# Kernel tuning notes

Hardware: AMD Instinct MI355X
Metric: run time of the kernel (lower is better)

Reference implementation:

```python
import jax, jax.numpy as jnp
import numpy as np

B, TQ, TK = 4, 128, 512
DQ = DK = DV = H = 1024


def setup_inputs() -> dict:
    key = jax.random.key(0)
    ks = jax.random.split(key, 7)
    s = 0.05  # keep tanh out of saturation
    return {
        "query": jax.random.normal(ks[0], (B, TQ, DQ), dtype=jnp.float32),
        "key": jax.random.normal(ks[1], (B, TK, DK), dtype=jnp.float32),
        "value": jax.random.normal(ks[2], (B, TK, DV), dtype=jnp.float32),
        "Wq": jax.random.normal(ks[3], (DQ, H), dtype=jnp.float32) * s,
        "bq": jax.random.normal(ks[4], (H,), dtype=jnp.float32) * s,
        "Wk": jax.random.normal(ks[5], (DK, H), dtype=jnp.float32) * s,
        "v": jax.random.normal(ks[6], (H,), dtype=jnp.float32) * s,
    }


def reference(query, key, value, Wq, bq, Wk, v):
    # additive (Bahdanau) attention
    wq = jnp.einsum("bqd,dh->bqh", query, Wq) + bq      # [B,Tq,H]
    uh = jnp.einsum("bkd,dh->bkh", key, Wk)             # [B,Tk,H]
    # broadcast add -> [B,Tq,Tk,H], tanh, project to scalar score
    scores = jnp.einsum("bqkh,h->bqk",
                        jnp.tanh(wq[:, :, None, :] + uh[:, None, :, :]), v)
    attn = jax.nn.softmax(scores, axis=-1)              # [B,Tq,Tk]
    h = jnp.einsum("bqk,bkv->bqv", attn, value)         # [B,Tq,Dv]
    return h, attn
```

## Files before the change

kernel.cpp:

```cpp
#include <hip/hip_runtime.h>
#include <hip/hip_bf16.h>

typedef float f32x4 __attribute__((ext_vector_type(4)));
typedef short s16x8 __attribute__((ext_vector_type(8)));
typedef short s16x4 __attribute__((ext_vector_type(4)));

#define NB  4
#define NTQ 128
#define NTK 512
#define NH  1024

__device__ __forceinline__ unsigned short f2bf(float x) {
    unsigned u = __builtin_bit_cast(unsigned, x);
    u += 0x7FFFu + ((u >> 16) & 1u);
    return (unsigned short)(u >> 16);
}

#define K2E  2.8853900817779268f

#define GLD16(gp, lp) __builtin_amdgcn_global_load_lds( \
    (const __attribute__((address_space(1))) unsigned int*)(gp), \
    (__attribute__((address_space(3))) unsigned int*)(lp), 16, 0, 0)

__global__ __launch_bounds__(256) void prep_kernel(
    const float* __restrict__ Q, const float* __restrict__ K,
    const float* __restrict__ Wq, const float* __restrict__ Wk,
    const float* __restrict__ value,
    short* __restrict__ Qb, short* __restrict__ Kb,
    short* __restrict__ WqT, short* __restrict__ WkT, short* __restrict__ valT)
{
    const int t = threadIdx.x, bx = blockIdx.x;
    if (bx < 2560) {
        const float* src; short* dst; size_t off;
        if (bx < 512) { src = Q; dst = Qb; off = (size_t)bx * 1024 + t * 4; }
        else          { src = K; dst = Kb; off = (size_t)(bx - 512) * 1024 + t * 4; }
        const float4 vv = *(const float4*)(src + off);
        s16x4 o = { (short)f2bf(vv.x), (short)f2bf(vv.y),
                    (short)f2bf(vv.z), (short)f2bf(vv.w) };
        *(s16x4*)(dst + off) = o;
        return;
    }
    __shared__ float tile[32][33];
    const float* src; short* dst; int R, C, r0, c0;
    if (bx < 3584)      { const int i = bx - 2560; src = Wq; dst = WqT; C = 1024; R = 1024; r0 = (i >> 5) * 32; c0 = (i & 31) * 32; }
    else if (bx < 4608) { const int i = bx - 3584; src = Wk; dst = WkT; C = 1024; R = 1024; r0 = (i >> 5) * 32; c0 = (i & 31) * 32; }
    else {
        const int i = bx - 4608, b = i >> 9, rr = i & 511;
        src = value + (size_t)b * 512 * 1024; dst = valT + (size_t)b * 1024 * 512;
        C = 1024; R = 512; r0 = (rr >> 5) * 32; c0 = (rr & 31) * 32;
    }
    const int lr = t >> 3, lc = (t & 7) * 4;
    {
        const float4 vv = *(const float4*)(src + (size_t)(r0 + lr) * C + c0 + lc);
        tile[lr][lc + 0] = vv.x; tile[lr][lc + 1] = vv.y;
        tile[lr][lc + 2] = vv.z; tile[lr][lc + 3] = vv.w;
    }
    __syncthreads();
    s16x4 o = { (short)f2bf(tile[lc + 0][lr]), (short)f2bf(tile[lc + 1][lr]),
                (short)f2bf(tile[lc + 2][lr]), (short)f2bf(tile[lc + 3][lr]) };
    *(s16x4*)(dst + (size_t)(c0 + lr) * R + r0 + lc) = o;
}

__global__ __launch_bounds__(256) void mm_kernel(
    const short* __restrict__ Qb, const short* __restrict__ Kb,
    const short* __restrict__ WqT, const short* __restrict__ WkT,
    const float* __restrict__ bq,
    float* __restrict__ Ea_out, float* __restrict__ EbT)
{
    __shared__ short lds[2][2][128][64];
    const int t = threadIdx.x, bx = blockIdx.x;
    const bool g1 = bx < 32;
    const short *A, *B; int m0, n0;
    if (g1) { A = Qb; B = WqT; m0 = (bx >> 3) * 128;        n0 = (bx & 7) * 128; }
    else    { const int i = bx - 32; A = Kb; B = WkT; m0 = (i >> 3) * 128; n0 = (i & 7) * 128; }
    A += (size_t)m0 * 1024; B += (size_t)n0 * 1024;

    f32x4 acc[4][4];
    #pragma unroll
    for (int i = 0; i < 4; ++i)
        #pragma unroll
        for (int j = 0; j < 4; ++j) acc[i][j] = f32x4{0.f, 0.f, 0.f, 0.f};

    const int lane = t & 63, wid = t >> 6;
    const int wr = wid >> 1, wc = wid & 1;
    const int fr = lane & 15, fko = (lane >> 4) * 16;

    #define STAGE_MM(buf, k0) do {                                              \
        _Pragma("unroll")                                                       \
        for (int it = 0; it < 4; ++it) {                                        \
            const int idx = it * 256 + t;                                       \
            const int row = idx >> 3, c16 = idx & 7;                            \
            const int sc = c16 ^ (row & 7);                                     \
            GLD16(A + (size_t)row * 1024 + (k0) + sc * 8,                       \
                  &lds[buf][0][0][0] + idx * 8);                                \
            GLD16(B + (size_t)row * 1024 + (k0) + sc * 8,                       \
                  &lds[buf][1][0][0] + idx * 8);                                \
        }                                                                       \
    } while (0)

    #define COMPUTE_MM(buf) do {                                                \
        _Pragma("unroll")                                                       \
        for (int kk = 0; kk < 2; ++kk) {                                        \
            s16x8 af[4], bfv[4];                                                \
            _Pragma("unroll")                                                   \
            for (int i = 0; i < 4; ++i) {                                       \
                const int rowA = wr * 64 + i * 16 + fr;                         \
                int offA = rowA * 128 + kk * 64 + fko; offA ^= (rowA & 7) << 4; \
                af[i] = *(const s16x8*)((const char*)&lds[buf][0][0][0] + offA);\
                const int rowB = wc * 64 + i * 16 + fr;                         \
                int offB = rowB * 128 + kk * 64 + fko; offB ^= (rowB & 7) << 4; \
                bfv[i] = *(const s16x8*)((const char*)&lds[buf][1][0][0] + offB);\
            }                                                                   \
            _Pragma("unroll")                                                   \
            for (int mi = 0; mi < 4; ++mi)                                      \
                _Pragma("unroll")                                               \
                for (int ni = 0; ni < 4; ++ni)                                  \
                    acc[mi][ni] = __builtin_amdgcn_mfma_f32_16x16x32_bf16(      \
                                      af[mi], bfv[ni], acc[mi][ni], 0, 0, 0);   \
        }                                                                       \
    } while (0)

    STAGE_MM(0, 0);
    __syncthreads();
    int cur = 0;
    for (int s = 0; s < 15; ++s) {
        STAGE_MM(cur ^ 1, (s + 1) * 64);
        COMPUTE_MM(cur);
        __syncthreads();
        cur ^= 1;
    }
    COMPUTE_MM(cur);

    const int row0 = (lane >> 4) * 4;
    if (g1) {
        #pragma unroll
        for (int ni = 0; ni < 4; ++ni) {
            const int n = n0 + wc * 64 + ni * 16 + fr;
            const float bias = bq[n];
            #pragma unroll
            for (int mi = 0; mi < 4; ++mi) {
                const int m = m0 + wr * 64 + mi * 16 + row0;
                #pragma unroll
                for (int j = 0; j < 4; ++j)
                    Ea_out[(size_t)(m + j) * 1024 + n] =
                        __builtin_amdgcn_exp2f(K2E * (acc[mi][ni][j] + bias));
            }
        }
    } else {
        #pragma unroll
        for (int mi = 0; mi < 4; ++mi) {
            const int m = m0 + wr * 64 + mi * 16 + row0;
            const int b = m >> 9, kk = m & 511;
            #pragma unroll
            for (int ni = 0; ni < 4; ++ni) {
                const int n = n0 + wc * 64 + ni * 16 + fr;
                f32x4 ev;
                #pragma unroll
                for (int j = 0; j < 4; ++j)
                    ev[j] = __builtin_amdgcn_exp2f(K2E * acc[mi][ni][j]);
                *(f32x4*)&EbT[((size_t)b * 1024 + n) * 512 + kk] = ev;
            }
        }
    }
    #undef STAGE_MM
    #undef COMPUTE_MM
}

__global__ __launch_bounds__(512) void scores_partial(
    const float* __restrict__ EbT, const float* __restrict__ Ea,
    const float* __restrict__ v, float* __restrict__ partial)
{
    __shared__ float s_ea[128][8];
    __shared__ float s_v[128];
    const int t = threadIdx.x, bx = blockIdx.x;
    const int hc = bx & 7, bq8 = bx >> 3;
    const int b = bq8 >> 4, q8 = bq8 & 15;
    const int bq0 = b * 128 + q8 * 8, h0 = hc * 128;

    if (t < 128) {
        #pragma unroll
        for (int q = 0; q < 8; ++q)
            s_ea[t][q] = Ea[(size_t)(bq0 + q) * 1024 + h0 + t];
        s_v[t] = v[h0 + t];
    }
    __syncthreads();

    const float* up = EbT + ((size_t)b * 1024 + h0) * 512 + t;
    float a[8] = {0.f, 0.f, 0.f, 0.f, 0.f, 0.f, 0.f, 0.f};
    #pragma unroll 4
    for (int hh = 0; hh < 128; ++hh) {
        const float eb = up[(size_t)hh * 512];
        const float vv = s_v[hh];
        #pragma unroll
        for (int q = 0; q < 8; ++q) {
            const float r = __builtin_amdgcn_rcpf(__builtin_fmaf(s_ea[hh][q], eb, 1.0f));
            a[q] = __builtin_fmaf(vv, r, a[q]);
        }
    }
    #pragma unroll
    for (int q = 0; q < 8; ++q)
        partial[((size_t)(bq0 + q) * 8 + hc) * 512 + t] = a[q];
}

__global__ __launch_bounds__(512) void softmax_kernel(
    const float* __restrict__ partial, float* __restrict__ attn_out,
    short* __restrict__ attnb)
{
    __shared__ float s_red[16];
    const int t = threadIdx.x, bqi = blockIdx.x;
    const float* p = partial + (size_t)bqi * 4096;
    float zs = 0.f;
    #pragma unroll
    for (int j = 0; j < 8; ++j) zs += p[j * 512 + t];
    const float z = -2.0f * zs;

    const int lane = t & 63, wid = t >> 6;
    float m = z;
    #pragma unroll
    for (int off = 32; off > 0; off >>= 1)
        m = fmaxf(m, __shfl_xor(m, off, 64));
    if (lane == 0) s_red[wid] = m;
    __syncthreads();
    if (t < 64) {
        float mm = (t < 8) ? s_red[t] : -3.0e38f;
        #pragma unroll
        for (int off = 4; off > 0; off >>= 1)
            mm = fmaxf(mm, __shfl_xor(mm, off, 64));
        if (t == 0) s_red[8] = mm;
    }
    __syncthreads();
    const float pr = __expf(z - s_red[8]);
    float s = pr;
    #pragma unroll
    for (int off = 32; off > 0; off >>= 1)
        s += __shfl_xor(s, off, 64);
    if (lane == 0) s_red[wid] = s;
    __syncthreads();
    if (t < 64) {
        float ss = (t < 8) ? s_red[t] : 0.f;
        #pragma unroll
        for (int off = 4; off > 0; off >>= 1)
            ss += __shfl_xor(ss, off, 64);
        if (t == 0) s_red[9] = ss;
    }
    __syncthreads();
    const float attn = pr * (1.0f / s_red[9]);
    attn_out[(size_t)bqi * 512 + t] = attn;
    attnb[(size_t)bqi * 512 + t] = (short)f2bf(attn);
}

__global__ __launch_bounds__(256) void pv_gemm(
    const short* __restrict__ attnb, const short* __restrict__ valT,
    float* __restrict__ outh)
{
    __shared__ short lds[2][2][128][64];
    const int t = threadIdx.x, bx = blockIdx.x;
    const int b = bx >> 3, nt = bx & 7;
    const int n0 = nt * 128;
    const short* A = attnb + (size_t)b * 128 * 512;
    const short* B = valT + (size_t)b * 1024 * 512 + (size_t)n0 * 512;

    f32x4 acc[4][4];
    #pragma unroll
    for (int i = 0; i < 4; ++i)
        #pragma unroll
        for (int j = 0; j < 4; ++j) acc[i][j] = f32x4{0.f, 0.f, 0.f, 0.f};

    const int lane = t & 63, wid = t >> 6;
    const int wr = wid >> 1, wc = wid & 1;
    const int fr = lane & 15, fko = (lane >> 4) * 16;

    #define STAGE_PV(buf, k0) do {                                              \
        _Pragma("unroll")                                                       \
        for (int it = 0; it < 4; ++it) {                                        \
            const int idx = it * 256 + t;                                       \
            const int row = idx >> 3, c16 = idx & 7;                            \
            const int sc = c16 ^ (row & 7);                                     \
            GLD16(A + (size_t)row * 512 + (k0) + sc * 8,                        \
                  &lds[buf][0][0][0] + idx * 8);                                \
            GLD16(B + (size_t)row * 512 + (k0) + sc * 8,                        \
                  &lds[buf][1][0][0] + idx * 8);                                \
        }                                                                       \
    } while (0)

    #define COMPUTE_PV(buf) do {                                                \
        _Pragma("unroll")                                                       \
        for (int kk = 0; kk < 2; ++kk) {                                        \
            s16x8 af[4], bfv[4];                                                \
            _Pragma("unroll")                                                   \
            for (int i = 0; i < 4; ++i) {                                       \
                const int rowA = wr * 64 + i * 16 + fr;                         \
                int offA = rowA * 128 + kk * 64 + fko; offA ^= (rowA & 7) << 4; \
                af[i] = *(const s16x8*)((const char*)&lds[buf][0][0][0] + offA);\
                const int rowB = wc * 64 + i * 16 + fr;                         \
                int offB = rowB * 128 + kk * 64 + fko; offB ^= (rowB & 7) << 4; \
                bfv[i] = *(const s16x8*)((const char*)&lds[buf][1][0][0] + offB);\
            }                                                                   \
            _Pragma("unroll")                                                   \
            for (int mi = 0; mi < 4; ++mi)                                      \
                _Pragma("unroll")                                               \
                for (int ni = 0; ni < 4; ++ni)                                  \
                    acc[mi][ni] = __builtin_amdgcn_mfma_f32_16x16x32_bf16(      \
                                      af[mi], bfv[ni], acc[mi][ni], 0, 0, 0);   \
        }                                                                       \
    } while (0)

    STAGE_PV(0, 0);
    __syncthreads();
    int cur = 0;
    for (int s = 0; s < 7; ++s) {
        STAGE_PV(cur ^ 1, (s + 1) * 64);
        COMPUTE_PV(cur);
        __syncthreads();
        cur ^= 1;
    }
    COMPUTE_PV(cur);

    const int row0 = (lane >> 4) * 4;
    #pragma unroll
    for (int ni = 0; ni < 4; ++ni) {
        const int n = n0 + wc * 64 + ni * 16 + fr;
        #pragma unroll
        for (int mi = 0; mi < 4; ++mi) {
            const int m = wr * 64 + mi * 16 + row0;
            #pragma unroll
            for (int j = 0; j < 4; ++j)
                outh[(size_t)(b * 128 + m + j) * 1024 + n] = acc[mi][ni][j];
        }
    }
    #undef STAGE_PV
    #undef COMPUTE_PV
}

extern "C" void kernel_launch(void* const* d_in, const int* in_sizes, int n_in,
                              void* d_out, int out_size, void* d_ws, size_t ws_size,
                              hipStream_t stream)
{
    const float* query = (const float*)d_in[0];
    const float* key   = (const float*)d_in[1];
    const float* value = (const float*)d_in[2];
    const float* Wq    = (const float*)d_in[3];
    const float* bq    = (const float*)d_in[4];
    const float* Wk    = (const float*)d_in[5];
    const float* v     = (const float*)d_in[6];
    float* out = (float*)d_out;

    char* w = (char*)d_ws;
    float* ws_Ea  = (float*)w;
    float* ws_EbT = (float*)(w + (2u << 20));
    char*  reg    = w + (10u << 20);
    short* Qb   = (short*)reg;
    short* Kb   = (short*)(reg + (1u << 20));
    short* WqT  = (short*)(reg + (5u << 20));
    short* WkT  = (short*)(reg + (7u << 20));
    float* part = (float*)reg;
    short* valT  = (short*)(w + (19u << 20));
    short* attnb = (short*)(w + (23u << 20));

    float* out_h    = out;
    float* out_attn = out + (size_t)NB * NTQ * NH;

    prep_kernel   <<<dim3(6656), dim3(256), 0, stream>>>(query, key, Wq, Wk, value,
                                                         Qb, Kb, WqT, WkT, valT);
    mm_kernel     <<<dim3(160),  dim3(256), 0, stream>>>(Qb, Kb, WqT, WkT, bq, ws_Ea, ws_EbT);
    scores_partial<<<dim3(512),  dim3(512), 0, stream>>>(ws_EbT, ws_Ea, v, part);
    softmax_kernel<<<dim3(512),  dim3(512), 0, stream>>>(part, out_attn, attnb);
    pv_gemm       <<<dim3(32),   dim3(256), 0, stream>>>(attnb, valT, out_h);
}
```

Measured before the change: 75.82 us.

## Halve GEMM N-tile to double block count, swizzle blocks, pack scores math

Both the projection GEMM and the PV GEMM switch from 128x128 to 128x64 output tiles, doubling the number of workgroups (160→320 and 32→64) to fill more of the CUs. The projection GEMM also remaps block indices across XCD-like groups of 8. The scores kernel packs the Ea values as float4 in shared memory and uses two-wide float vectors for the fma and accumulate so packed FP32 instructions can be used. Smaller tiles lower per-block data reuse and add global traffic for the A operand.

```diff
diff --git a/kernel.cpp b/kernel.cpp
--- a/kernel.cpp
+++ b/kernel.cpp
@@ -2,6 +2,7 @@
 #include <hip/hip_bf16.h>
 
 typedef float f32x4 __attribute__((ext_vector_type(4)));
+typedef float f32x2 __attribute__((ext_vector_type(2)));
 typedef short s16x8 __attribute__((ext_vector_type(8)));
 typedef short s16x4 __attribute__((ext_vector_type(4)));
 
@@ -67,19 +68,22 @@
     const float* __restrict__ bq,
     float* __restrict__ Ea_out, float* __restrict__ EbT)
 {
-    __shared__ short lds[2][2][128][64];
-    const int t = threadIdx.x, bx = blockIdx.x;
-    const bool g1 = bx < 32;
+    __shared__ short ldsA[2][128][64];
+    __shared__ short ldsB[2][64][64];
+    const int t = threadIdx.x;
+    const int bx0 = blockIdx.x;
+    const int bx = (bx0 & 7) * 40 + (bx0 >> 3);
+    const bool g1 = bx < 64;
     const short *A, *B; int m0, n0;
-    if (g1) { A = Qb; B = WqT; m0 = (bx >> 3) * 128;        n0 = (bx & 7) * 128; }
-    else    { const int i = bx - 32; A = Kb; B = WkT; m0 = (i >> 3) * 128; n0 = (i & 7) * 128; }
+    if (g1) { A = Qb; B = WqT; m0 = (bx >> 4) * 128; n0 = (bx & 15) * 64; }
+    else    { const int i = bx - 64; A = Kb; B = WkT; m0 = (i >> 4) * 128; n0 = (i & 15) * 64; }
     A += (size_t)m0 * 1024; B += (size_t)n0 * 1024;
 
-    f32x4 acc[4][4];
+    f32x4 acc[4][2];
     #pragma unroll
     for (int i = 0; i < 4; ++i)
         #pragma unroll
-        for (int j = 0; j < 4; ++j) acc[i][j] = f32x4{0.f, 0.f, 0.f, 0.f};
+        for (int j = 0; j < 2; ++j) acc[i][j] = f32x4{0.f, 0.f, 0.f, 0.f};
 
     const int lane = t & 63, wid = t >> 6;
     const int wr = wid >> 1, wc = wid & 1;
@@ -92,29 +96,38 @@
             const int row = idx >> 3, c16 = idx & 7;                            \
             const int sc = c16 ^ (row & 7);                                     \
             GLD16(A + (size_t)row * 1024 + (k0) + sc * 8,                       \
-                  &lds[buf][0][0][0] + idx * 8);                                \
+                  &ldsA[buf][0][0] + idx * 8);                                  \
+        }                                                                       \
+        _Pragma("unroll")                                                       \
+        for (int it = 0; it < 2; ++it) {                                        \
+            const int idx = it * 256 + t;                                       \
+            const int row = idx >> 3, c16 = idx & 7;                            \
+            const int sc = c16 ^ (row & 7);                                     \
             GLD16(B + (size_t)row * 1024 + (k0) + sc * 8,                       \
-                  &lds[buf][1][0][0] + idx * 8);                                \
+                  &ldsB[buf][0][0] + idx * 8);                                  \
         }                                                                       \
     } while (0)
 
     #define COMPUTE_MM(buf) do {                                                \
         _Pragma("unroll")                                                       \
         for (int kk = 0; kk < 2; ++kk) {                                        \
-            s16x8 af[4], bfv[4];                                                \
+            s16x8 af[4], bfv[2];                                                \
             _Pragma("unroll")                                                   \
             for (int i = 0; i < 4; ++i) {                                       \
                 const int rowA = wr * 64 + i * 16 + fr;                         \
                 int offA = rowA * 128 + kk * 64 + fko; offA ^= (rowA & 7) << 4; \
-                af[i] = *(const s16x8*)((const char*)&lds[buf][0][0][0] + offA);\
-                const int rowB = wc * 64 + i * 16 + fr;                         \
+                af[i] = *(const s16x8*)((const char*)&ldsA[buf][0][0] + offA);  \
+            }                                                                   \
+            _Pragma("unroll")                                                   \
+            for (int ni = 0; ni < 2; ++ni) {                                    \
+                const int rowB = wc * 32 + ni * 16 + fr;                        \
                 int offB = rowB * 128 + kk * 64 + fko; offB ^= (rowB & 7) << 4; \
-                bfv[i] = *(const s16x8*)((const char*)&lds[buf][1][0][0] + offB);\
+                bfv[ni] = *(const s16x8*)((const char*)&ldsB[buf][0][0] + offB);\
             }                                                                   \
             _Pragma("unroll")                                                   \
             for (int mi = 0; mi < 4; ++mi)                                      \
                 _Pragma("unroll")                                               \
-                for (int ni = 0; ni < 4; ++ni)                                  \
+                for (int ni = 0; ni < 2; ++ni)                                  \
                     acc[mi][ni] = __builtin_amdgcn_mfma_f32_16x16x32_bf16(      \
                                       af[mi], bfv[ni], acc[mi][ni], 0, 0, 0);   \
         }                                                                       \
@@ -134,8 +147,8 @@
     const int row0 = (lane >> 4) * 4;
     if (g1) {
         #pragma unroll
-        for (int ni = 0; ni < 4; ++ni) {
-            const int n = n0 + wc * 64 + ni * 16 + fr;
+        for (int ni = 0; ni < 2; ++ni) {
+            const int n = n0 + wc * 32 + ni * 16 + fr;
             const float bias = bq[n];
             #pragma unroll
             for (int mi = 0; mi < 4; ++mi) {
@@ -152,8 +165,8 @@
             const int m = m0 + wr * 64 + mi * 16 + row0;
             const int b = m >> 9, kk = m & 511;
             #pragma unroll
-            for (int ni = 0; ni < 4; ++ni) {
-                const int n = n0 + wc * 64 + ni * 16 + fr;
+            for (int ni = 0; ni < 2; ++ni) {
+                const int n = n0 + wc * 32 + ni * 16 + fr;
                 f32x4 ev;
                 #pragma unroll
                 for (int j = 0; j < 4; ++j)
@@ -170,36 +183,56 @@
     const float* __restrict__ EbT, const float* __restrict__ Ea,
     const float* __restrict__ v, float* __restrict__ partial)
 {
-    __shared__ float s_ea[128][8];
-    __shared__ float s_v[128];
+    __shared__ float4 s_ea4[128][2];
+    __shared__ float  s_v[128];
     const int t = threadIdx.x, bx = blockIdx.x;
     const int hc = bx & 7, bq8 = bx >> 3;
     const int b = bq8 >> 4, q8 = bq8 & 15;
     const int bq0 = b * 128 + q8 * 8, h0 = hc * 128;
 
     if (t < 128) {
-        #pragma unroll
-        for (int q = 0; q < 8; ++q)
-            s_ea[t][q] = Ea[(size_t)(bq0 + q) * 1024 + h0 + t];
-        s_v[t] = v[h0 + t];
+        const int h = h0 + t;
+        s_ea4[t][0] = make_float4(Ea[(size_t)(bq0 + 0) * 1024 + h],
+                                  Ea[(size_t)(bq0 + 1) * 1024 + h],
+                                  Ea[(size_t)(bq0 + 2) * 1024 + h],
+                                  Ea[(size_t)(bq0 + 3) * 1024 + h]);
+        s_ea4[t][1] = make_float4(Ea[(size_t)(bq0 + 4) * 1024 + h],
+                                  Ea[(size_t)(bq0 + 5) * 1024 + h],
+                                  Ea[(size_t)(bq0 + 6) * 1024 + h],
+                                  Ea[(size_t)(bq0 + 7) * 1024 + h]);
+        s_v[t] = v[h];
     }
     __syncthreads();
 
     const float* up = EbT + ((size_t)b * 1024 + h0) * 512 + t;
-    float a[8] = {0.f, 0.f, 0.f, 0.f, 0.f, 0.f, 0.f, 0.f};
+    f32x2 a0 = {0.f, 0.f}, a1 = {0.f, 0.f}, a2 = {0.f, 0.f}, a3 = {0.f, 0.f};
     #pragma unroll 4
     for (int hh = 0; hh < 128; ++hh) {
-        const float eb = up[(size_t)hh * 512];
-        const float vv = s_v[hh];
-        #pragma unroll
-        for (int q = 0; q < 8; ++q) {
-            const float r = __builtin_amdgcn_rcpf(__builtin_fmaf(s_ea[hh][q], eb, 1.0f));
-            a[q] = __builtin_fmaf(vv, r, a[q]);
-        }
-    }
-    #pragma unroll
-    for (int q = 0; q < 8; ++q)
-        partial[((size_t)(bq0 + q) * 8 + hc) * 512 + t] = a[q];
+        const float  eb = up[(size_t)hh * 512];
+        const float4 e0 = s_ea4[hh][0];
+        const float4 e1 = s_ea4[hh][1];
+        const float  vv = s_v[hh];
+        f32x2 p0 = f32x2{e0.x, e0.y} * eb + 1.0f;
+        f32x2 p1 = f32x2{e0.z, e0.w} * eb + 1.0f;
+        f32x2 p2 = f32x2{e1.x, e1.y} * eb + 1.0f;
+        f32x2 p3 = f32x2{e1.z, e1.w} * eb + 1.0f;
+        f32x2 r0 = {__builtin_amdgcn_rcpf(p0.x), __builtin_amdgcn_rcpf(p0.y)};
+        f32x2 r1 = {__builtin_amdgcn_rcpf(p1.x), __builtin_amdgcn_rcpf(p1.y)};
+        f32x2 r2 = {__builtin_amdgcn_rcpf(p2.x), __builtin_amdgcn_rcpf(p2.y)};
+        f32x2 r3 = {__builtin_amdgcn_rcpf(p3.x), __builtin_amdgcn_rcpf(p3.y)};
+        a0 += r0 * vv;
+        a1 += r1 * vv;
+        a2 += r2 * vv;
+        a3 += r3 * vv;
+    }
+    partial[((size_t)(bq0 + 0) * 8 + hc) * 512 + t] = a0.x;
+    partial[((size_t)(bq0 + 1) * 8 + hc) * 512 + t] = a0.y;
+    partial[((size_t)(bq0 + 2) * 8 + hc) * 512 + t] = a1.x;
+    partial[((size_t)(bq0 + 3) * 8 + hc) * 512 + t] = a1.y;
+    partial[((size_t)(bq0 + 4) * 8 + hc) * 512 + t] = a2.x;
+    partial[((size_t)(bq0 + 5) * 8 + hc) * 512 + t] = a2.y;
+    partial[((size_t)(bq0 + 6) * 8 + hc) * 512 + t] = a3.x;
+    partial[((size_t)(bq0 + 7) * 8 + hc) * 512 + t] = a3.y;
 }
 
 __global__ __launch_bounds__(512) void softmax_kernel(
@@ -253,18 +286,19 @@
     const short* __restrict__ attnb, const short* __restrict__ valT,
     float* __restrict__ outh)
 {
-    __shared__ short lds[2][2][128][64];
+    __shared__ short ldsA[2][128][64];
+    __shared__ short ldsB[2][64][64];
     const int t = threadIdx.x, bx = blockIdx.x;
-    const int b = bx >> 3, nt = bx & 7;
-    const int n0 = nt * 128;
+    const int b = bx >> 4, nt = bx & 15;
+    const int n0 = nt * 64;
     const short* A = attnb + (size_t)b * 128 * 512;
     const short* B = valT + (size_t)b * 1024 * 512 + (size_t)n0 * 512;
 
-    f32x4 acc[4][4];
+    f32x4 acc[4][2];
     #pragma unroll
     for (int i = 0; i < 4; ++i)
         #pragma unroll
-        for (int j = 0; j < 4; ++j) acc[i][j] = f32x4{0.f, 0.f, 0.f, 0.f};
+        for (int j = 0; j < 2; ++j) acc[i][j] = f32x4{0.f, 0.f, 0.f, 0.f};
 
     const int lane = t & 63, wid = t >> 6;
     const int wr = wid >> 1, wc = wid & 1;
@@ -277,29 +311,38 @@
             const int row = idx >> 3, c16 = idx & 7;                            \
             const int sc = c16 ^ (row & 7);                                     \
             GLD16(A + (size_t)row * 512 + (k0) + sc * 8,                        \
-                  &lds[buf][0][0][0] + idx * 8);                                \
+                  &ldsA[buf][0][0] + idx * 8);                                  \
+        }                                                                       \
+        _Pragma("unroll")                                                       \
+        for (int it = 0; it < 2; ++it) {                                        \
+            const int idx = it * 256 + t;                                       \
+            const int row = idx >> 3, c16 = idx & 7;                            \
+            const int sc = c16 ^ (row & 7);                                     \
             GLD16(B + (size_t)row * 512 + (k0) + sc * 8,                        \
-                  &lds[buf][1][0][0] + idx * 8);                                \
+                  &ldsB[buf][0][0] + idx * 8);                                  \
         }                                                                       \
     } while (0)
 
     #define COMPUTE_PV(buf) do {                                                \
         _Pragma("unroll")                                                       \
         for (int kk = 0; kk < 2; ++kk) {                                        \
-            s16x8 af[4], bfv[4];                                                \
+            s16x8 af[4], bfv[2];                                                \
             _Pragma("unroll")                                                   \
             for (int i = 0; i < 4; ++i) {                                       \
                 const int rowA = wr * 64 + i * 16 + fr;                         \
                 int offA = rowA * 128 + kk * 64 + fko; offA ^= (rowA & 7) << 4; \
-                af[i] = *(const s16x8*)((const char*)&lds[buf][0][0][0] + offA);\
-                const int rowB = wc * 64 + i * 16 + fr;                         \
+                af[i] = *(const s16x8*)((const char*)&ldsA[buf][0][0] + offA);  \
+            }                                                                   \
+            _Pragma("unroll")                                                   \
+            for (int ni = 0; ni < 2; ++ni) {                                    \
+                const int rowB = wc * 32 + ni * 16 + fr;                        \
                 int offB = rowB * 128 + kk * 64 + fko; offB ^= (rowB & 7) << 4; \
-                bfv[i] = *(const s16x8*)((const char*)&lds[buf][1][0][0] + offB);\
+                bfv[ni] = *(const s16x8*)((const char*)&ldsB[buf][0][0] + offB);\
             }                                                                   \
             _Pragma("unroll")                                                   \
             for (int mi = 0; mi < 4; ++mi)                                      \
                 _Pragma("unroll")                                               \
-                for (int ni = 0; ni < 4; ++ni)                                  \
+                for (int ni = 0; ni < 2; ++ni)                                  \
                     acc[mi][ni] = __builtin_amdgcn_mfma_f32_16x16x32_bf16(      \
                                       af[mi], bfv[ni], acc[mi][ni], 0, 0, 0);   \
         }                                                                       \
@@ -318,8 +361,8 @@
 
     const int row0 = (lane >> 4) * 4;
     #pragma unroll
-    for (int ni = 0; ni < 4; ++ni) {
-        const int n = n0 + wc * 64 + ni * 16 + fr;
+    for (int ni = 0; ni < 2; ++ni) {
+        const int n = n0 + wc * 32 + ni * 16 + fr;
         #pragma unroll
         for (int mi = 0; mi < 4; ++mi) {
             const int m = wr * 64 + mi * 16 + row0;
@@ -362,8 +405,8 @@
 
     prep_kernel   <<<dim3(6656), dim3(256), 0, stream>>>(query, key, Wq, Wk, value,
                                                          Qb, Kb, WqT, WkT, valT);
-    mm_kernel     <<<dim3(160),  dim3(256), 0, stream>>>(Qb, Kb, WqT, WkT, bq, ws_Ea, ws_EbT);
+    mm_kernel     <<<dim3(320),  dim3(256), 0, stream>>>(Qb, Kb, WqT, WkT, bq, ws_Ea, ws_EbT);
     scores_partial<<<dim3(512),  dim3(512), 0, stream>>>(ws_EbT, ws_Ea, v, part);
     softmax_kernel<<<dim3(512),  dim3(512), 0, stream>>>(part, out_attn, attnb);
-    pv_gemm       <<<dim3(32),   dim3(256), 0, stream>>>(attnb, valT, out_h);
-}
+    pv_gemm       <<<dim3(64),   dim3(256), 0, stream>>>(attnb, valT, out_h);
+}
```

New measurement: 76.01 us. About the same (+0.3%).
